# Kernel optimization log

Hardware: AMD Instinct MI355X
Metric: run time of the kernel (lower is better)

Reference implementation:

```python
import jax, jax.numpy as jnp
import numpy as np

DIM = 1024
N_HEADS = 16
HEAD_DIM = DIM // N_HEADS
SCALE = HEAD_DIM ** -0.5


def setup_inputs() -> dict:
    key = jax.random.key(0)
    ks = jax.random.split(key, 10)
    B, L, L_low = 4, 4096, 1024
    s = DIM ** -0.5
    return {
        "x_broad": jax.random.normal(ks[0], (B, L, DIM), jnp.float32),
        "x_low": jax.random.normal(ks[1], (B, L_low, DIM), jnp.float32),
        "Wq": jax.random.normal(ks[2], (DIM, DIM), jnp.float32) * s,
        "bq": jnp.zeros((DIM,), jnp.float32),
        "Wk": jax.random.normal(ks[3], (DIM, DIM), jnp.float32) * s,
        "bk": jnp.zeros((DIM,), jnp.float32),
        "Wv": jax.random.normal(ks[4], (DIM, DIM), jnp.float32) * s,
        "bv": jnp.zeros((DIM,), jnp.float32),
        "Wo": jax.random.normal(ks[5], (DIM, DIM), jnp.float32) * s,
        "bo": jnp.zeros((DIM,), jnp.float32),
    }


def reference(x_broad, x_low, Wq, bq, Wk, bk, Wv, bv, Wo, bo):
    B, L, D = x_broad.shape
    Ll = x_low.shape[1]
    # projections (torch Linear: x @ W.T + b)
    q = (x_broad @ Wq.T + bq).reshape(B, L, N_HEADS, HEAD_DIM)
    k = (x_low @ Wk.T + bk).reshape(B, Ll, N_HEADS, HEAD_DIM)
    v = (x_low @ Wv.T + bv).reshape(B, Ll, N_HEADS, HEAD_DIM)
    # scores: [B, H, L, L_low]
    attn = jnp.einsum("blhd,bmhd->bhlm", q, k) * SCALE
    attn = jax.nn.softmax(attn, axis=-1)
    out = jnp.einsum("bhlm,bmhd->blhd", attn, v).reshape(B, L, D)
    return out @ Wo.T + bo
```

## Files before the change

kernel.cpp:

```cpp
#include <hip/hip_runtime.h>
#include <hip/hip_bf16.h>

typedef __bf16 bf16;
typedef __bf16 bf16x4 __attribute__((ext_vector_type(4)));
typedef __bf16 bf16x8 __attribute__((ext_vector_type(8)));
typedef float f32x4 __attribute__((ext_vector_type(4)));

#define MFMA16(a, b, c) __builtin_amdgcn_mfma_f32_16x16x32_bf16(a, b, c, 0, 0, 0)

constexpr int DIM = 1024;
constexpr int NH = 16;
constexpr int HD = 64;
constexpr float SCALE = 0.125f;
constexpr float L2E = 1.4426950408889634f;
constexpr float SCL2E = SCALE * L2E;

__device__ __forceinline__ float fast_exp2(float x) {
  float r;
  asm("v_exp_f32 %0, %1" : "=v"(r) : "v"(x));
  return r;
}

__device__ __forceinline__ void gl_lds16(const void* g, void* l) {
  __builtin_amdgcn_global_load_lds((const __attribute__((address_space(1))) void*)g,
                                   (__attribute__((address_space(3))) void*)l, 16, 0, 0);
}

__global__ __launch_bounds__(256) void cvt_f32_bf16(const float* __restrict__ s,
                                                    bf16* __restrict__ d, int n8) {
  const int i = blockIdx.x * 256 + threadIdx.x;
  if (i < n8) {
    const float4 v0 = ((const float4*)s)[i * 2];
    const float4 v1 = ((const float4*)s)[i * 2 + 1];
    bf16x8 o = {(bf16)v0.x, (bf16)v0.y, (bf16)v0.z, (bf16)v0.w,
                (bf16)v1.x, (bf16)v1.y, (bf16)v1.z, (bf16)v1.w};
    ((bf16x8*)d)[i] = o;
  }
}

__global__ __launch_bounds__(256) void cvt_w4(const float* __restrict__ a,
                                              const float* __restrict__ b,
                                              const float* __restrict__ c,
                                              const float* __restrict__ d,
                                              bf16* __restrict__ o) {
  constexpr int N8 = DIM * DIM / 8;
  const int i = blockIdx.x * 256 + threadIdx.x;
  const int g = i >> 17;
  const int j = i & (N8 - 1);
  const float* s = (g == 0) ? a : (g == 1) ? b : (g == 2) ? c : d;
  const float4 v0 = ((const float4*)s)[j * 2];
  const float4 v1 = ((const float4*)s)[j * 2 + 1];
  bf16x8 ov = {(bf16)v0.x, (bf16)v0.y, (bf16)v0.z, (bf16)v0.w,
               (bf16)v1.x, (bf16)v1.y, (bf16)v1.z, (bf16)v1.w};
  ((bf16x8*)o)[i] = ov;
}

template <int OUT_MODE>
__global__ __launch_bounds__(256) void gemm_bf16(const bf16* __restrict__ A,
                                                 const bf16* __restrict__ W,
                                                 const float* __restrict__ bias,
                                                 void* __restrict__ Cptr, int Lq,
                                                 float oscale) {
  __shared__ bf16 As[128 * 64];
  __shared__ bf16 Bs[128 * 64];

  const int bm = blockIdx.x * 128;
  const int bn = blockIdx.y * 128;
  const int tid = threadIdx.x;
  const int w = tid >> 6;
  const int lane = tid & 63;
  const int quad = lane >> 4;
  const int l16 = lane & 15;
  const int wm = (w >> 1) * 64;
  const int wn = (w & 1) * 64;
  const int lr = lane >> 3;
  const int sc8 = (((lane & 7) ^ lr)) << 3;
  const int x7 = l16 & 7;

  size_t aOff[4], bOff[4];
#pragma unroll
  for (int r = 0; r < 4; ++r) {
    const int rowt = (r * 4 + w) * 8 + lr;
    aOff[r] = (size_t)(bm + rowt) * DIM + sc8;
    bOff[r] = (size_t)(bn + rowt) * DIM + sc8;
  }

  f32x4 acc[4][4] = {};

  for (int k0 = 0; k0 < DIM; k0 += 64) {
#pragma unroll
    for (int r = 0; r < 4; ++r) {
      gl_lds16(A + aOff[r] + k0, (char*)As + (r * 4 + w) * 1024);
      gl_lds16(W + bOff[r] + k0, (char*)Bs + (r * 4 + w) * 1024);
    }
    __syncthreads();

#pragma unroll
    for (int s = 0; s < 2; ++s) {
      bf16x8 af[4], bfr[4];
#pragma unroll
      for (int mi = 0; mi < 4; ++mi)
        af[mi] = *(const bf16x8*)((char*)As + (wm + mi * 16 + l16) * 128 +
                                  (((quad + 4 * s) ^ x7) << 4));
#pragma unroll
      for (int ni = 0; ni < 4; ++ni)
        bfr[ni] = *(const bf16x8*)((char*)Bs + (wn + ni * 16 + l16) * 128 +
                                   (((quad + 4 * s) ^ x7) << 4));
#pragma unroll
      for (int mi = 0; mi < 4; ++mi)
#pragma unroll
        for (int ni = 0; ni < 4; ++ni)
          acc[mi][ni] = MFMA16(af[mi], bfr[ni], acc[mi][ni]);
    }
    __syncthreads();
  }

#pragma unroll
  for (int mi = 0; mi < 4; ++mi) {
#pragma unroll
    for (int ni = 0; ni < 4; ++ni) {
      const int col = bn + wn + ni * 16 + l16;
      const float bv = bias[col];
#pragma unroll
      for (int r = 0; r < 4; ++r) {
        const int row = bm + wm + mi * 16 + quad * 4 + r;
        const float val = (acc[mi][ni][r] + bv) * oscale;
        if constexpr (OUT_MODE == 0) {
          ((float*)Cptr)[(size_t)row * DIM + col] = val;
        } else if constexpr (OUT_MODE == 1) {
          const int b = row / Lq;
          const int l = row - b * Lq;
          ((bf16*)Cptr)[((size_t)((b * NH + (col >> 6)) * Lq + l) << 6) + (col & 63)] =
              (bf16)val;
        } else {
          const int b = row >> 10;
          const int kv = row & 1023;
          ((bf16*)Cptr)[(((size_t)(b * NH + (col >> 6)) << 6) + (col & 63)) * 1024 + kv] =
              (bf16)val;
        }
      }
    }
  }
}

template <int OUT_MODE, bool A_BF16>
__global__ __launch_bounds__(256) void gemm_nt(const void* __restrict__ Aptr,
                                               const float* __restrict__ W,
                                               const float* __restrict__ bias,
                                               void* __restrict__ Cptr, int Lq,
                                               float oscale) {
  constexpr int LDT = 72;
  __shared__ bf16 As[128 * LDT];
  __shared__ bf16 Bs[128 * LDT];

  const int bm = blockIdx.x * 128;
  const int bn = blockIdx.y * 128;
  const int tid = threadIdx.x;
  const int w = tid >> 6;
  const int lane = tid & 63;
  const int quad = lane >> 4;
  const int l16 = lane & 15;
  const int wm = (w >> 1) * 64;
  const int wn = (w & 1) * 64;

  f32x4 acc[4][4] = {};

  for (int k0 = 0; k0 < DIM; k0 += 64) {
#pragma unroll
    for (int i = 0; i < 8; ++i) {
      int f = i * 256 + tid;
      int row = f >> 4;
      int c4 = (f & 15) << 2;
      const float4 v = *(const float4*)(W + (size_t)(bn + row) * DIM + k0 + c4);
      bf16x4 bv = {(bf16)v.x, (bf16)v.y, (bf16)v.z, (bf16)v.w};
      *(bf16x4*)&Bs[row * LDT + c4] = bv;
    }
    if constexpr (A_BF16) {
      const bf16* Ab = (const bf16*)Aptr;
#pragma unroll
      for (int i = 0; i < 4; ++i) {
        int f = i * 256 + tid;
        int row = f >> 3;
        int c8 = (f & 7) << 3;
        *(bf16x8*)&As[row * LDT + c8] =
            *(const bf16x8*)(Ab + (size_t)(bm + row) * DIM + k0 + c8);
      }
    } else {
      const float* Af = (const float*)Aptr;
#pragma unroll
      for (int i = 0; i < 8; ++i) {
        int f = i * 256 + tid;
        int row = f >> 4;
        int c4 = (f & 15) << 2;
        const float4 v = *(const float4*)(Af + (size_t)(bm + row) * DIM + k0 + c4);
        bf16x4 av = {(bf16)v.x, (bf16)v.y, (bf16)v.z, (bf16)v.w};
        *(bf16x4*)&As[row * LDT + c4] = av;
      }
    }
    __syncthreads();

#pragma unroll
    for (int sub = 0; sub < 2; ++sub) {
      bf16x8 af[4], bfr[4];
#pragma unroll
      for (int mi = 0; mi < 4; ++mi)
        af[mi] = *(const bf16x8*)&As[(wm + mi * 16 + l16) * LDT + sub * 32 + quad * 8];
#pragma unroll
      for (int ni = 0; ni < 4; ++ni)
        bfr[ni] = *(const bf16x8*)&Bs[(wn + ni * 16 + l16) * LDT + sub * 32 + quad * 8];
#pragma unroll
      for (int mi = 0; mi < 4; ++mi)
#pragma unroll
        for (int ni = 0; ni < 4; ++ni)
          acc[mi][ni] = MFMA16(af[mi], bfr[ni], acc[mi][ni]);
    }
    __syncthreads();
  }

#pragma unroll
  for (int mi = 0; mi < 4; ++mi) {
#pragma unroll
    for (int ni = 0; ni < 4; ++ni) {
      const int col = bn + wn + ni * 16 + l16;
      const float bv = bias[col];
#pragma unroll
      for (int r = 0; r < 4; ++r) {
        const int row = bm + wm + mi * 16 + quad * 4 + r;
        const float val = (acc[mi][ni][r] + bv) * oscale;
        if constexpr (OUT_MODE == 0) {
          ((float*)Cptr)[(size_t)row * DIM + col] = val;
        } else if constexpr (OUT_MODE == 1) {
          const int b = row / Lq;
          const int l = row - b * Lq;
          ((bf16*)Cptr)[((size_t)((b * NH + (col >> 6)) * Lq + l) << 6) + (col & 63)] =
              (bf16)val;
        } else {
          const int b = row >> 10;
          const int kv = row & 1023;
          ((bf16*)Cptr)[(((size_t)(b * NH + (col >> 6)) << 6) + (col & 63)) * 1024 + kv] =
              (bf16)val;
        }
      }
    }
  }
}

__global__ __launch_bounds__(256) void attn_fused(const bf16* __restrict__ Q,
                                                  const bf16* __restrict__ K,
                                                  const bf16* __restrict__ VT,
                                                  bf16* __restrict__ O) {
  constexpr int LDP = 72;
  __shared__ bf16 Ks[2][64 * 64];
  __shared__ bf16 Vs[2][64 * 64];
  __shared__ bf16 Ps[4 * 2 * 16 * LDP];

  const int qt = blockIdx.x;
  const int h = blockIdx.y;
  const int b = blockIdx.z;
  const int tid = threadIdx.x;
  const int w = tid >> 6;
  const int lane = tid & 63;
  const int quad = lane >> 4;
  const int l16 = lane & 15;
  const int lr = lane >> 3;
  const int sc8 = (((lane & 7) ^ lr)) << 3;
  const int x7 = l16 & 7;

  const bf16* Qp = Q + ((size_t)(b * NH + h) * 4096 + qt * 128 + w * 32 + l16) * HD + quad * 8;
  const bf16* Kb = K + (size_t)(b * NH + h) * 1024 * HD;
  const bf16* Vb = VT + (size_t)(b * NH + h) * HD * 1024;

  bf16x8 qf[2][2];
#pragma unroll
  for (int g = 0; g < 2; ++g)
#pragma unroll
    for (int s = 0; s < 2; ++s) qf[g][s] = *(const bf16x8*)(Qp + g * 16 * HD + s * 32);

  bf16* pw0 = &Ps[(w * 2 + 0) * 16 * LDP];
  bf16* pw1 = &Ps[(w * 2 + 1) * 16 * LDP];

  f32x4 oacc[2][4] = {};
  f32x4 ls[2] = {};

  auto stage = [&](int kt, int bi) {
#pragma unroll
    for (int c2 = 0; c2 < 2; ++c2) {
      const int c = c2 * 4 + w;
      gl_lds16(Kb + (size_t)(kt + c * 8 + lr) * HD + sc8, (char*)&Ks[bi][0] + c * 1024);
      gl_lds16(Vb + (size_t)(c * 8 + lr) * 1024 + kt + sc8, (char*)&Vs[bi][0] + c * 1024);
    }
  };

  stage(0, 0);
  int buf = 0;
  for (int kt = 0; kt < 1024; kt += 64) {
    __syncthreads();
    if (kt + 64 < 1024) stage(kt + 64, buf ^ 1);

    bf16x8 kf[4][2];
#pragma unroll
    for (int nt = 0; nt < 4; ++nt)
#pragma unroll
      for (int s = 0; s < 2; ++s)
        kf[nt][s] = *(const bf16x8*)((char*)&Ks[buf][0] + (nt * 16 + l16) * 128 +
                                     (((quad + 4 * s) ^ x7) << 4));

#pragma unroll
    for (int g = 0; g < 2; ++g) {
      bf16* pw = g ? pw1 : pw0;
      f32x4 psum = {0.f, 0.f, 0.f, 0.f};
#pragma unroll
      for (int nt = 0; nt < 4; ++nt) {
        f32x4 a = {0.f, 0.f, 0.f, 0.f};
        a = MFMA16(kf[nt][0], qf[g][0], a);
        a = MFMA16(kf[nt][1], qf[g][1], a);
        bf16x4 pb;
#pragma unroll
        for (int r = 0; r < 4; ++r) {
          const float p = fast_exp2(a[r]);
          psum[r] += p;
          pb[r] = (bf16)p;
        }
        *(bf16x4*)(pw + l16 * LDP + nt * 16 + quad * 4) = pb;
      }
      ls[g] += psum;
    }

    bf16x8 pf[2][2];
#pragma unroll
    for (int g = 0; g < 2; ++g) {
      const bf16* pw = g ? pw1 : pw0;
#pragma unroll
      for (int s = 0; s < 2; ++s)
        pf[g][s] = *(const bf16x8*)(pw + l16 * LDP + s * 32 + quad * 8);
    }

#pragma unroll
    for (int dt = 0; dt < 4; ++dt) {
      bf16x8 vf0 = *(const bf16x8*)((char*)&Vs[buf][0] + (dt * 16 + l16) * 128 +
                                    ((quad ^ x7) << 4));
      bf16x8 vf1 = *(const bf16x8*)((char*)&Vs[buf][0] + (dt * 16 + l16) * 128 +
                                    ((((quad + 4)) ^ x7) << 4));
      oacc[0][dt] = MFMA16(vf0, pf[0][0], oacc[0][dt]);
      oacc[0][dt] = MFMA16(vf1, pf[0][1], oacc[0][dt]);
      oacc[1][dt] = MFMA16(vf0, pf[1][0], oacc[1][dt]);
      oacc[1][dt] = MFMA16(vf1, pf[1][1], oacc[1][dt]);
    }
    buf ^= 1;
  }

  float lq0 = ls[0][0] + ls[0][1] + ls[0][2] + ls[0][3];
  float lq1 = ls[1][0] + ls[1][1] + ls[1][2] + ls[1][3];
  lq0 += __shfl_xor(lq0, 16);
  lq0 += __shfl_xor(lq0, 32);
  lq1 += __shfl_xor(lq1, 16);
  lq1 += __shfl_xor(lq1, 32);
  const float inv[2] = {1.f / lq0, 1.f / lq1};

#pragma unroll
  for (int g = 0; g < 2; ++g) {
    const size_t orow =
        ((size_t)(b * 4096 + qt * 128 + w * 32 + g * 16 + l16)) * DIM + h * 64;
#pragma unroll
    for (int dt = 0; dt < 4; ++dt) {
      bf16x4 ov = {(bf16)(oacc[g][dt][0] * inv[g]), (bf16)(oacc[g][dt][1] * inv[g]),
                   (bf16)(oacc[g][dt][2] * inv[g]), (bf16)(oacc[g][dt][3] * inv[g])};
      *(bf16x4*)(O + orow + dt * 16 + quad * 4) = ov;
    }
  }
}

extern "C" void kernel_launch(void* const* d_in, const int* in_sizes, int n_in,
                              void* d_out, int out_size, void* d_ws, size_t ws_size,
                              hipStream_t stream) {
  const float* x_broad = (const float*)d_in[0];
  const float* x_low = (const float*)d_in[1];
  const float* Wq = (const float*)d_in[2];
  const float* bq = (const float*)d_in[3];
  const float* Wk = (const float*)d_in[4];
  const float* bk = (const float*)d_in[5];
  const float* Wv = (const float*)d_in[6];
  const float* bv = (const float*)d_in[7];
  const float* Wo = (const float*)d_in[8];
  const float* bo = (const float*)d_in[9];

  constexpr int B = 4, L = 4096, LL = 1024;
  const size_t qBytes = (size_t)B * NH * L * HD * 2;
  const size_t kvBytes = (size_t)B * NH * LL * HD * 2;
  const size_t oBytes = qBytes;
  const size_t xlBytes = kvBytes;
  const size_t wBytes = (size_t)DIM * DIM * 2;

  char* ws = (char*)d_ws;
  bf16* Qw = (bf16*)ws;
  bf16* Kw = (bf16*)(ws + qBytes);
  bf16* Vw = (bf16*)(ws + qBytes + kvBytes);
  bf16* Ow = (bf16*)(ws + qBytes + 2 * kvBytes);

  const dim3 blk(256);
  const size_t need = qBytes + 2 * kvBytes + oBytes + xlBytes + 4 * wBytes;

  if (ws_size >= need) {
    bf16* xbB = Ow;
    bf16* xlB = (bf16*)(ws + qBytes + 2 * kvBytes + oBytes);
    bf16* WqB = (bf16*)(ws + qBytes + 2 * kvBytes + oBytes + xlBytes);
    bf16* WkB = WqB + (size_t)DIM * DIM;
    bf16* WvB = WkB + (size_t)DIM * DIM;
    bf16* WoB = WvB + (size_t)DIM * DIM;

    hipLaunchKernelGGL(cvt_f32_bf16, dim3(B * L * DIM / 8 / 256), blk, 0, stream,
                       x_broad, xbB, B * L * DIM / 8);
    hipLaunchKernelGGL(cvt_f32_bf16, dim3(B * LL * DIM / 8 / 256), blk, 0, stream,
                       x_low, xlB, B * LL * DIM / 8);
    hipLaunchKernelGGL(cvt_w4, dim3(4 * DIM * DIM / 8 / 256), blk, 0, stream, Wq, Wk,
                       Wv, Wo, WqB);

    hipLaunchKernelGGL((gemm_bf16<1>), dim3(B * L / 128, DIM / 128), blk, 0, stream,
                       xbB, WqB, bq, Qw, L, SCL2E);
    hipLaunchKernelGGL((gemm_bf16<1>), dim3(B * LL / 128, DIM / 128), blk, 0, stream,
                       xlB, WkB, bk, Kw, LL, 1.0f);
    hipLaunchKernelGGL((gemm_bf16<2>), dim3(B * LL / 128, DIM / 128), blk, 0, stream,
                       xlB, WvB, bv, Vw, LL, 1.0f);
    hipLaunchKernelGGL(attn_fused, dim3(L / 128, NH, B), blk, 0, stream, Qw, Kw, Vw, Ow);
    hipLaunchKernelGGL((gemm_bf16<0>), dim3(B * L / 128, DIM / 128), blk, 0, stream,
                       Ow, WoB, bo, d_out, 1, 1.0f);
  } else {
    hipLaunchKernelGGL((gemm_nt<1, false>), dim3(B * L / 128, DIM / 128), blk, 0,
                       stream, x_broad, Wq, bq, Qw, L, SCL2E);
    hipLaunchKernelGGL((gemm_nt<1, false>), dim3(B * LL / 128, DIM / 128), blk, 0,
                       stream, x_low, Wk, bk, Kw, LL, 1.0f);
    hipLaunchKernelGGL((gemm_nt<2, false>), dim3(B * LL / 128, DIM / 128), blk, 0,
                       stream, x_low, Wv, bv, Vw, LL, 1.0f);
    hipLaunchKernelGGL(attn_fused, dim3(L / 128, NH, B), blk, 0, stream, Qw, Kw, Vw, Ow);
    hipLaunchKernelGGL((gemm_nt<0, true>), dim3(B * L / 128, DIM / 128), blk, 0,
                       stream, Ow, Wo, bo, d_out, 1, 1.0f);
  }
}
```

Baseline: 374.5 us.

## Compute softmax row sums via ones-MFMA, swizzle P buffer, add setprio

The per-element fp32 accumulation of exp values is replaced by an MFMA of a ones vector against the bf16 P fragments, so the row sum comes from the matrix unit instead of VALU adds and cross-lane shuffles. The P scratch buffer is shrunk to one 16x64 tile per wave, reused for both query groups, with an XOR swizzle replacing the padding. s_setprio hints are placed around the MFMA phases. The row sums now use bf16-rounded probabilities, which slightly changes numerics, and reusing the single P buffer adds a dependency between the two groups.

```diff
diff --git a/kernel.cpp b/kernel.cpp
--- a/kernel.cpp
+++ b/kernel.cpp
@@ -249,10 +249,9 @@
                                                   const bf16* __restrict__ K,
                                                   const bf16* __restrict__ VT,
                                                   bf16* __restrict__ O) {
-  constexpr int LDP = 72;
   __shared__ bf16 Ks[2][64 * 64];
   __shared__ bf16 Vs[2][64 * 64];
-  __shared__ bf16 Ps[4 * 2 * 16 * LDP];
+  __shared__ bf16 Ps[4 * 16 * 64];
 
   const int qt = blockIdx.x;
   const int h = blockIdx.y;
@@ -276,11 +275,14 @@
 #pragma unroll
     for (int s = 0; s < 2; ++s) qf[g][s] = *(const bf16x8*)(Qp + g * 16 * HD + s * 32);
 
-  bf16* pw0 = &Ps[(w * 2 + 0) * 16 * LDP];
-  bf16* pw1 = &Ps[(w * 2 + 1) * 16 * LDP];
+  char* pw = (char*)&Ps[w * 16 * 64];
 
   f32x4 oacc[2][4] = {};
-  f32x4 ls[2] = {};
+  f32x4 lacc[2] = {};
+
+  bf16x8 ones;
+#pragma unroll
+  for (int i = 0; i < 8; ++i) ones[i] = (bf16)1.0f;
 
   auto stage = [&](int kt, int bi) {
 #pragma unroll
@@ -305,10 +307,10 @@
         kf[nt][s] = *(const bf16x8*)((char*)&Ks[buf][0] + (nt * 16 + l16) * 128 +
                                      (((quad + 4 * s) ^ x7) << 4));
 
+    bf16x8 pf[2][2];
 #pragma unroll
     for (int g = 0; g < 2; ++g) {
-      bf16* pw = g ? pw1 : pw0;
-      f32x4 psum = {0.f, 0.f, 0.f, 0.f};
+      __builtin_amdgcn_s_setprio(1);
 #pragma unroll
       for (int nt = 0; nt < 4; ++nt) {
         f32x4 a = {0.f, 0.f, 0.f, 0.f};
@@ -316,25 +318,18 @@
         a = MFMA16(kf[nt][1], qf[g][1], a);
         bf16x4 pb;
 #pragma unroll
-        for (int r = 0; r < 4; ++r) {
-          const float p = fast_exp2(a[r]);
-          psum[r] += p;
-          pb[r] = (bf16)p;
-        }
-        *(bf16x4*)(pw + l16 * LDP + nt * 16 + quad * 4) = pb;
+        for (int r = 0; r < 4; ++r) pb[r] = (bf16)fast_exp2(a[r]);
+        *(bf16x4*)(pw + l16 * 128 + ((nt * 32 + quad * 8) ^ (x7 << 4))) = pb;
       }
-      ls[g] += psum;
-    }
-
-    bf16x8 pf[2][2];
-#pragma unroll
-    for (int g = 0; g < 2; ++g) {
-      const bf16* pw = g ? pw1 : pw0;
+      __builtin_amdgcn_s_setprio(0);
 #pragma unroll
       for (int s = 0; s < 2; ++s)
-        pf[g][s] = *(const bf16x8*)(pw + l16 * LDP + s * 32 + quad * 8);
-    }
-
+        pf[g][s] = *(const bf16x8*)(pw + l16 * 128 + ((s * 64 + quad * 16) ^ (x7 << 4)));
+      lacc[g] = MFMA16(ones, pf[g][0], lacc[g]);
+      lacc[g] = MFMA16(ones, pf[g][1], lacc[g]);
+    }
+
+    __builtin_amdgcn_s_setprio(1);
 #pragma unroll
     for (int dt = 0; dt < 4; ++dt) {
       bf16x8 vf0 = *(const bf16x8*)((char*)&Vs[buf][0] + (dt * 16 + l16) * 128 +
@@ -346,16 +341,11 @@
       oacc[1][dt] = MFMA16(vf0, pf[1][0], oacc[1][dt]);
       oacc[1][dt] = MFMA16(vf1, pf[1][1], oacc[1][dt]);
     }
+    __builtin_amdgcn_s_setprio(0);
     buf ^= 1;
   }
 
-  float lq0 = ls[0][0] + ls[0][1] + ls[0][2] + ls[0][3];
-  float lq1 = ls[1][0] + ls[1][1] + ls[1][2] + ls[1][3];
-  lq0 += __shfl_xor(lq0, 16);
-  lq0 += __shfl_xor(lq0, 32);
-  lq1 += __shfl_xor(lq1, 16);
-  lq1 += __shfl_xor(lq1, 32);
-  const float inv[2] = {1.f / lq0, 1.f / lq1};
+  const float inv[2] = {1.f / lacc[0][0], 1.f / lacc[1][0]};
 
 #pragma unroll
   for (int g = 0; g < 2; ++g) {
```

After: 372.5 us. Within noise of the previous version (-0.5%).
